# Optimization experiments

Hardware: AMD Instinct MI355X
Metric: run time of the kernel (lower is better)

Reference implementation:

```python
import jax, jax.numpy as jnp
import numpy as np

NQ = 10          # qubits per register
DIM = 2 ** NQ    # 1024 amplitudes
N_CLS = 10       # canonical images (one per class)
N = 16384        # batch of samples
IMG = 28 * 28    # 784 pixels, zero-padded to DIM


def setup_inputs() -> dict:
    key = jax.random.key(0)
    k1, k2, k3 = jax.random.split(key, 3)
    z_re = jax.random.normal(k1, (N, DIM), dtype=jnp.float32)
    z_im = jax.random.normal(k2, (N, DIM), dtype=jnp.float32)
    # inputs are quantum states -> L2-normalize the complex vectors
    nrm = jnp.sqrt(jnp.sum(z_re * z_re + z_im * z_im, axis=1, keepdims=True))
    z_re = z_re / nrm
    z_im = z_im / nrm
    canon = jax.random.uniform(k3, (N_CLS, 1, 28, 28), dtype=jnp.float32)
    return {"z_re": z_re, "z_im": z_im, "canon": canon}


def reference(z_re, z_im, canon):
    # reshape_norm_padding: flatten, zero-pad to 2^nq, L2-normalize (real amplitudes)
    ref = canon.reshape(N_CLS, IMG)
    ref = jnp.pad(ref, ((0, 0), (0, DIM - IMG)))                  # [C, DIM]
    ref = ref / jnp.linalg.norm(ref, axis=1, keepdims=True)
    # Swap test: <Z_anc> = |<val|ref>|^2. ref is real, so with val = z_re + i*z_im:
    #   <val|ref> = (z_re @ ref^T) - i*(z_im @ ref^T)
    s_re = jnp.einsum('nd,cd->nc', z_re, ref)                     # [N, C]
    s_im = jnp.einsum('nd,cd->nc', z_im, ref)                     # [N, C]
    return s_re * s_re + s_im * s_im                              # [N, C] float32
```

## Files before the change

kernel.cpp:

```cpp
#include <hip/hip_runtime.h>

#define DIM     1024
#define N_CLS   10
#define NROWS   16384
#define IMG     784

#define NF4      196
#define NF4_PAD  208
#define NSTEP    13
#define LSTRIDE  208

#define ROWS_PER_BLK 16

typedef float f32x4 __attribute__((ext_vector_type(4)));
typedef float f32x2 __attribute__((ext_vector_type(2)));

static __device__ __forceinline__ f32x2 lo2(f32x4 v) {
  return __builtin_shufflevector(v, v, 0, 1);
}
static __device__ __forceinline__ f32x2 hi2(f32x4 v) {
  return __builtin_shufflevector(v, v, 2, 3);
}

static __device__ __forceinline__ void pk_fma(f32x2& acc, f32x2 a, f32x2 b) {
  asm("v_pk_fma_f32 %0, %1, %2, %0" : "+v"(acc) : "v"(a), "v"(b));
}

__device__ __forceinline__ float wave64_sum(float x) {
#define DPP_ADD(ctrl, rmask, bmask)                                           \
  x += __int_as_float(__builtin_amdgcn_update_dpp(                            \
      0, __float_as_int(x), ctrl, rmask, bmask, true));
  DPP_ADD(0x111, 0xf, 0xf)
  DPP_ADD(0x112, 0xf, 0xf)
  DPP_ADD(0x114, 0xf, 0xe)
  DPP_ADD(0x118, 0xf, 0xc)
  DPP_ADD(0x142, 0xa, 0xf)
  DPP_ADD(0x143, 0xc, 0xf)
#undef DPP_ADD
  return x;
}

__device__ __forceinline__ float group16_sum(float x) {
#define DPP_ADD(ctrl)                                                         \
  x += __int_as_float(__builtin_amdgcn_update_dpp(                            \
      0, __float_as_int(x), ctrl, 0xf, 0xf, true));
  DPP_ADD(0x111)
  DPP_ADD(0x112)
  DPP_ADD(0x114)
  DPP_ADD(0x118)
#undef DPP_ADD
  return x;
}

__global__ __launch_bounds__(256, 4) void swaptest_kernel(
    const float* __restrict__ zre, const float* __restrict__ zim,
    const float* __restrict__ canon, float* __restrict__ out) {
  __shared__ f32x4 lref[N_CLS * LSTRIDE];

  const int t = threadIdx.x;
  const int lane = t & 63;
  const int wave = t >> 6;

#pragma unroll
  for (int c = 0; c < N_CLS; ++c) {
    if (t < NF4_PAD) {
      f32x4 v = {0.f, 0.f, 0.f, 0.f};
      if (t < NF4) v = ((const f32x4*)canon)[c * NF4 + t];
      lref[c * LSTRIDE + t] = v;
    }
  }
  __syncthreads();

  for (int c = wave; c < N_CLS; c += 4) {
    float ss = 0.f;
    for (int i = lane; i < NF4_PAD; i += 64) {
      f32x4 v = lref[c * LSTRIDE + i];
      ss += v.x * v.x + v.y * v.y + v.z * v.z + v.w * v.w;
    }
    ss = wave64_sum(ss);
    float inv = __shfl(1.0f / sqrtf(ss), 63);
    for (int i = lane; i < NF4_PAD; i += 64) {
      f32x4 v = lref[c * LSTRIDE + i];
      v.x *= inv; v.y *= inv; v.z *= inv; v.w *= inv;
      lref[c * LSTRIDE + i] = v;
    }
  }
  __syncthreads();

  const int s = lane & 15;
  const int g = lane >> 4;
  const int row = blockIdx.x * ROWS_PER_BLK + wave * 4 + g;

  const f32x4* pr = (const f32x4*)(zre + ((size_t)row << 10)) + s;
  const f32x4* pi = (const f32x4*)(zim + ((size_t)row << 10)) + s;

  f32x2 accr[N_CLS], acci[N_CLS];
#pragma unroll
  for (int c = 0; c < N_CLS; ++c) {
    accr[c] = (f32x2){0.f, 0.f};
    acci[c] = (f32x2){0.f, 0.f};
  }

  f32x4 zr_n = pr[0];
  f32x4 zi_n = pi[0];
#pragma unroll
  for (int j = 0; j < NSTEP; ++j) {
    const f32x4 zr = zr_n;
    const f32x4 zi = zi_n;
    if (j + 1 < NSTEP) {
      zr_n = pr[(j + 1) * 16];
      zi_n = pi[(j + 1) * 16];
    }
#pragma unroll
    for (int c = 0; c < N_CLS; ++c) {
      const f32x4 rv = lref[c * LSTRIDE + j * 16 + s];
      pk_fma(accr[c], lo2(zr), lo2(rv));
      pk_fma(accr[c], hi2(zr), hi2(rv));
      pk_fma(acci[c], lo2(zi), lo2(rv));
      pk_fma(acci[c], hi2(zi), hi2(rv));
    }
  }

#pragma unroll
  for (int c = 0; c < N_CLS; ++c) {
    float sr = group16_sum(accr[c].x + accr[c].y);
    float si = group16_sum(acci[c].x + acci[c].y);
    if (s == 15) {
      out[(size_t)row * N_CLS + c] = sr * sr + si * si;
    }
  }
}

extern "C" void kernel_launch(void* const* d_in, const int* in_sizes, int n_in,
                              void* d_out, int out_size, void* d_ws,
                              size_t ws_size, hipStream_t stream) {
  const float* z_re = (const float*)d_in[0];
  const float* z_im = (const float*)d_in[1];
  const float* canon = (const float*)d_in[2];
  float* out = (float*)d_out;
  (void)d_ws; (void)ws_size;

  const int nblk = NROWS / ROWS_PER_BLK;
  swaptest_kernel<<<nblk, 256, 0, stream>>>(z_re, z_im, canon, out);
}
```

Baseline: 149.3 us.

## Use 32 lanes per row and 512-thread blocks for the swap-test dot products

Each row is now reduced by 32 lanes instead of 16, so every lane handles 7 float4 steps instead of 13. Blocks grow to 8 waves of 512 threads, with 16 rows still processed per block. The LDS reference table is padded to 224 float4s and the last step's loads are masked for the upper half of the lanes. The intent is more memory parallelism per row and a shorter serial loop per lane. In exchange it drops the explicit software prefetch, adds one DPP reduction stage, and spends wasted lanes in the final partial step.

```diff
diff --git a/kernel.cpp b/kernel.cpp
--- a/kernel.cpp
+++ b/kernel.cpp
@@ -6,11 +6,12 @@
 #define IMG     784
 
 #define NF4      196
-#define NF4_PAD  208
-#define NSTEP    13
-#define LSTRIDE  208
+#define NF4_PAD  224
+#define NSTEP    7
+#define LSTRIDE  224
 
-#define ROWS_PER_BLK 16
+#define WAVES_PER_BLK 8
+#define ROWS_PER_BLK  16
 
 typedef float f32x4 __attribute__((ext_vector_type(4)));
 typedef float f32x2 __attribute__((ext_vector_type(2)));
@@ -26,33 +27,31 @@
   asm("v_pk_fma_f32 %0, %1, %2, %0" : "+v"(acc) : "v"(a), "v"(b));
 }
 
-__device__ __forceinline__ float wave64_sum(float x) {
 #define DPP_ADD(ctrl, rmask, bmask)                                           \
   x += __int_as_float(__builtin_amdgcn_update_dpp(                            \
       0, __float_as_int(x), ctrl, rmask, bmask, true));
+
+__device__ __forceinline__ float wave64_sum(float x) {
   DPP_ADD(0x111, 0xf, 0xf)
   DPP_ADD(0x112, 0xf, 0xf)
   DPP_ADD(0x114, 0xf, 0xe)
   DPP_ADD(0x118, 0xf, 0xc)
   DPP_ADD(0x142, 0xa, 0xf)
   DPP_ADD(0x143, 0xc, 0xf)
-#undef DPP_ADD
   return x;
 }
 
-__device__ __forceinline__ float group16_sum(float x) {
-#define DPP_ADD(ctrl)                                                         \
-  x += __int_as_float(__builtin_amdgcn_update_dpp(                            \
-      0, __float_as_int(x), ctrl, 0xf, 0xf, true));
-  DPP_ADD(0x111)
-  DPP_ADD(0x112)
-  DPP_ADD(0x114)
-  DPP_ADD(0x118)
-#undef DPP_ADD
+__device__ __forceinline__ float group32_sum(float x) {
+  DPP_ADD(0x111, 0xf, 0xf)
+  DPP_ADD(0x112, 0xf, 0xf)
+  DPP_ADD(0x114, 0xf, 0xe)
+  DPP_ADD(0x118, 0xf, 0xc)
+  DPP_ADD(0x142, 0xa, 0xf)
   return x;
 }
+#undef DPP_ADD
 
-__global__ __launch_bounds__(256, 4) void swaptest_kernel(
+__global__ __launch_bounds__(512, 8) void swaptest_kernel(
     const float* __restrict__ zre, const float* __restrict__ zim,
     const float* __restrict__ canon, float* __restrict__ out) {
   __shared__ f32x4 lref[N_CLS * LSTRIDE];
@@ -71,7 +70,7 @@
   }
   __syncthreads();
 
-  for (int c = wave; c < N_CLS; c += 4) {
+  for (int c = wave; c < N_CLS; c += WAVES_PER_BLK) {
     float ss = 0.f;
     for (int i = lane; i < NF4_PAD; i += 64) {
       f32x4 v = lref[c * LSTRIDE + i];
@@ -87,9 +86,9 @@
   }
   __syncthreads();
 
-  const int s = lane & 15;
-  const int g = lane >> 4;
-  const int row = blockIdx.x * ROWS_PER_BLK + wave * 4 + g;
+  const int s = lane & 31;
+  const int g = lane >> 5;
+  const int row = blockIdx.x * ROWS_PER_BLK + wave * 2 + g;
 
   const f32x4* pr = (const f32x4*)(zre + ((size_t)row << 10)) + s;
   const f32x4* pi = (const f32x4*)(zim + ((size_t)row << 10)) + s;
@@ -101,19 +100,17 @@
     acci[c] = (f32x2){0.f, 0.f};
   }
 
-  f32x4 zr_n = pr[0];
-  f32x4 zi_n = pi[0];
 #pragma unroll
   for (int j = 0; j < NSTEP; ++j) {
-    const f32x4 zr = zr_n;
-    const f32x4 zi = zi_n;
-    if (j + 1 < NSTEP) {
-      zr_n = pr[(j + 1) * 16];
-      zi_n = pi[(j + 1) * 16];
+    f32x4 zr = {0.f, 0.f, 0.f, 0.f};
+    f32x4 zi = {0.f, 0.f, 0.f, 0.f};
+    if (j < NSTEP - 1 || s < 16) {
+      zr = pr[j * 32];
+      zi = pi[j * 32];
     }
 #pragma unroll
     for (int c = 0; c < N_CLS; ++c) {
-      const f32x4 rv = lref[c * LSTRIDE + j * 16 + s];
+      const f32x4 rv = lref[c * LSTRIDE + j * 32 + s];
       pk_fma(accr[c], lo2(zr), lo2(rv));
       pk_fma(accr[c], hi2(zr), hi2(rv));
       pk_fma(acci[c], lo2(zi), lo2(rv));
@@ -123,9 +120,9 @@
 
 #pragma unroll
   for (int c = 0; c < N_CLS; ++c) {
-    float sr = group16_sum(accr[c].x + accr[c].y);
-    float si = group16_sum(acci[c].x + acci[c].y);
-    if (s == 15) {
+    float sr = group32_sum(accr[c].x + accr[c].y);
+    float si = group32_sum(acci[c].x + acci[c].y);
+    if (s == 31) {
       out[(size_t)row * N_CLS + c] = sr * sr + si * si;
     }
   }
@@ -141,5 +138,5 @@
   (void)d_ws; (void)ws_size;
 
   const int nblk = NROWS / ROWS_PER_BLK;
-  swaptest_kernel<<<nblk, 256, 0, stream>>>(z_re, z_im, canon, out);
+  swaptest_kernel<<<nblk, 512, 0, stream>>>(z_re, z_im, canon, out);
 }
```

Result: slower. 153.8 us (+3.0%).
